# Kernel tuning notes

Measured on AMD Instinct MI355X. Metric: run time of the kernel, lower is better.

The kernel has to match this reference:

```python
import jax, jax.numpy as jnp
import numpy as np

B, H, M_DIM, K, N = 4, 8, 2048, 2048, 64
NNZ = B * H * M_DIM * 64


def setup_inputs() -> dict:
    key = jax.random.key(0)
    k_val, k_b, k_bh, k_m, k_k = jax.random.split(key, 5)
    values = jax.random.normal(k_val, (NNZ,), dtype=jnp.float32)
    b = jax.random.normal(k_b, (B, H, K, N), dtype=jnp.float32)
    idx_bh = jax.random.randint(k_bh, (NNZ,), 0, B * H, dtype=jnp.int32)
    idx_m = jax.random.randint(k_m, (NNZ,), 0, M_DIM, dtype=jnp.int32)
    idx_k = jax.random.randint(k_k, (NNZ,), 0, K, dtype=jnp.int32)
    return {"values": values, "b": b, "idx_bh": idx_bh, "idx_m": idx_m,
            "idx_k": idx_k, "M": M_DIM}


def reference(values, b, idx_bh, idx_m, idx_k, M):
    # Batched sparse-dense matmul: out[b,h,m,:] = sum_k A[b,h,m,k] * b[b,h,k,:]
    # A is in COO form over flattened batch-head dim: (idx_bh, idx_m, idx_k, values).
    Bd, Hd, Kd, Nd = b.shape
    b_flat = b.reshape(Bd * Hd, Kd, Nd)             # [BH, K, N]
    # gather the dense rows each nonzero touches, scale by the sparse value
    gathered = values[:, None] * b_flat[idx_bh, idx_k]  # [nnz, N]
    # scatter-add into output rows (flat segment id = bh*M + m)
    seg = idx_bh * M + idx_m
    out = jax.ops.segment_sum(gathered, seg, num_segments=Bd * Hd * M)  # [BH*M, N]
    return out.reshape(Bd, Hd, M, Nd)
```

## Files before the change

kernel.cpp:

```cpp
#include <hip/hip_runtime.h>

constexpr int N_COLS = 64;
constexpr int K_DIM  = 2048;
constexpr int M_DIM  = 2048;
constexpr int SEGS   = 32 * 2048;
constexpr int NBUCK  = 512;
constexpr int SEG_PER_BUCK = SEGS / NBUCK;
constexpr int PART_T = 512;
constexpr int PART_E = 16;
constexpr int TILE   = PART_T * PART_E;
constexpr int CAP2   = 8192;
constexpr int CSTR   = 16;
constexpr int OVL_CAP = 640;
constexpr size_t OVFCNT_OFF = 32768;
constexpr size_t OVFBUF_OFF = 40960;
constexpr int OVF_GCAP = (int)((524288 - OVFBUF_OFF) / 8);

struct Pair { float v; int k; };

__global__ void spmm_coo_atomic(const float* __restrict__ values,
                                const float* __restrict__ b,
                                const int*   __restrict__ idx_bh,
                                const int*   __restrict__ idx_m,
                                const int*   __restrict__ idx_k,
                                float*       __restrict__ out,
                                int nnz) {
    long long gid = (long long)blockIdx.x * blockDim.x + threadIdx.x;
    int nz   = (int)(gid >> 6);
    int lane = (int)(gid & 63);
    if (nz >= nnz) return;
    float bval = b[((size_t)idx_bh[nz] * K_DIM + idx_k[nz]) * N_COLS + lane];
    atomicAdd(&out[((size_t)idx_bh[nz] * M_DIM + idx_m[nz]) * N_COLS + lane],
              values[nz] * bval);
}

__global__ __launch_bounds__(PART_T)
void partition512(const float* __restrict__ values,
                  const int*   __restrict__ idx_bh,
                  const int*   __restrict__ idx_m,
                  const int*   __restrict__ idx_k,
                  int*  __restrict__ cursor,
                  int*  __restrict__ ovfcnt,
                  Pair* __restrict__ ovf,
                  Pair* __restrict__ packed, int nnz) {
    __shared__ int2 ebuf[TILE];
    __shared__ int lcount[NBUCK];
    __shared__ int sc[NBUCK];
    __shared__ int lstart[NBUCK];
    __shared__ int total_s;

    int t = threadIdx.x;
    lcount[t] = 0;
    __syncthreads();

    int e0 = blockIdx.x * TILE + t * PART_E;
    float v[PART_E];
    int   pk[PART_E];
    short bkt[PART_E];
    short rnk[PART_E];

    if (e0 + PART_E <= nnz) {
        const float4* vv4 = (const float4*)(values + e0);
        const int4*   bh4 = (const int4*)(idx_bh + e0);
        const int4*   mm4 = (const int4*)(idx_m + e0);
        const int4*   kk4 = (const int4*)(idx_k + e0);
        #pragma unroll
        for (int q = 0; q < PART_E / 4; ++q) {
            float4 vq = vv4[q];
            int4   bq = bh4[q], mq = mm4[q], kq = kk4[q];
            int s0 = bq.x * M_DIM + mq.x;
            int s1 = bq.y * M_DIM + mq.y;
            int s2 = bq.z * M_DIM + mq.z;
            int s3 = bq.w * M_DIM + mq.w;
            int b0 = s0 >> 7, b1 = s1 >> 7, b2 = s2 >> 7, b3 = s3 >> 7;
            v[4*q+0]=vq.x; pk[4*q+0]=(kq.x<<8)|((s0&127)<<19)|(b0&0xFF)|((b0>>8)<<26);
            bkt[4*q+0]=(short)b0; rnk[4*q+0]=(short)atomicAdd(&lcount[b0],1);
            v[4*q+1]=vq.y; pk[4*q+1]=(kq.y<<8)|((s1&127)<<19)|(b1&0xFF)|((b1>>8)<<26);
            bkt[4*q+1]=(short)b1; rnk[4*q+1]=(short)atomicAdd(&lcount[b1],1);
            v[4*q+2]=vq.z; pk[4*q+2]=(kq.z<<8)|((s2&127)<<19)|(b2&0xFF)|((b2>>8)<<26);
            bkt[4*q+2]=(short)b2; rnk[4*q+2]=(short)atomicAdd(&lcount[b2],1);
            v[4*q+3]=vq.w; pk[4*q+3]=(kq.w<<8)|((s3&127)<<19)|(b3&0xFF)|((b3>>8)<<26);
            bkt[4*q+3]=(short)b3; rnk[4*q+3]=(short)atomicAdd(&lcount[b3],1);
        }
    } else {
        #pragma unroll
        for (int i = 0; i < PART_E; ++i) {
            int e = e0 + i;
            if (e < nnz) {
                int seg = idx_bh[e] * M_DIM + idx_m[e];
                int bu  = seg >> 7;
                v[i]  = values[e];
                pk[i] = (idx_k[e] << 8) | ((seg & 127) << 19)
                      | (bu & 0xFF) | ((bu >> 8) << 26);
                bkt[i] = (short)bu;
                rnk[i] = (short)atomicAdd(&lcount[bu], 1);
            } else bkt[i] = -1;
        }
    }
    __syncthreads();

    int c = lcount[t];
    int sbase = (c > 0) ? atomicAdd(&cursor[t * CSTR], c) : 0;

    sc[t] = c;
    __syncthreads();
    for (int d = 1; d < NBUCK; d <<= 1) {
        int x = (t >= d) ? sc[t - d] : 0;
        __syncthreads();
        sc[t] += x;
        __syncthreads();
    }
    int ls = sc[t] - c;
    lstart[t] = ls;
    if (t == NBUCK - 1) total_s = sc[t];
    __syncthreads();
    sc[t] = sbase - ls;

    #pragma unroll
    for (int i = 0; i < PART_E; ++i) {
        if (bkt[i] >= 0)
            ebuf[lstart[bkt[i]] + rnk[i]] = make_int2(__float_as_int(v[i]), pk[i]);
    }
    __syncthreads();

    int total = total_s;
    for (int p = t; p < total; p += PART_T) {
        int2 e = ebuf[p];
        int bu = (e.y & 0xFF) | ((e.y >> 18) & 0x100);
        int gpos = sc[bu] + p;
        if (gpos < CAP2) {
            *(int2*)&packed[(size_t)bu * CAP2 + gpos] = e;
        } else {
            int o = atomicAdd(ovfcnt, 1);
            if (o < OVF_GCAP) *(int2*)&ovf[o] = e;
        }
    }
}

__global__ __launch_bounds__(1024)
void sort_accum(const Pair* __restrict__ packed,
                const int*  __restrict__ cursor,
                const int*  __restrict__ ovfcnt,
                const Pair* __restrict__ ovf,
                const float* __restrict__ b,
                float* __restrict__ out) {
    __shared__ int2 ps[CAP2 + OVL_CAP + 8];
    __shared__ int2 ovl[OVL_CAP];
    __shared__ int h[SEG_PER_BUCK];
    __shared__ int cur[SEG_PER_BUCK];
    __shared__ int ovl_n;

    int t = threadIdx.x;
    int i   = blockIdx.x;
    int bkt = (i & 7) * 64 + (i >> 3);
    int cnt = cursor[bkt * CSTR];
    int L = cnt;
    if (L < 0)    L = 0;
    if (L > CAP2) L = CAP2;

    if (t < SEG_PER_BUCK) h[t] = 0;
    if (t == 0) ovl_n = 0;
    __syncthreads();

    const int2* src = (const int2*)(packed + (size_t)bkt * CAP2);
    int2 reg[8];
    #pragma unroll
    for (int q = 0; q < 8; ++q) {
        int idx = t + q * 1024;
        if (idx < L) {
            reg[q] = src[idx];
            atomicAdd(&h[(reg[q].y >> 19) & 127], 1);
        }
    }
    int ovfN = ovfcnt[0];
    if (ovfN > OVF_GCAP) ovfN = OVF_GCAP;
    const int2* osrc = (const int2*)ovf;
    for (int o = t; o < ovfN; o += 1024) {
        int2 e = osrc[o];
        int eb = (e.y & 0xFF) | ((e.y >> 18) & 0x100);
        if (eb == bkt) {
            int pos = atomicAdd(&ovl_n, 1);
            if (pos < OVL_CAP) {
                ovl[pos] = e;
                atomicAdd(&h[(e.y >> 19) & 127], 1);
            }
        }
    }
    __syncthreads();

    for (int d = 1; d < SEG_PER_BUCK; d <<= 1) {
        int x = 0;
        if (t < SEG_PER_BUCK && t >= d) x = h[t - d];
        __syncthreads();
        if (t < SEG_PER_BUCK && t >= d) h[t] += x;
        __syncthreads();
    }
    if (t < SEG_PER_BUCK) cur[t] = (t == 0) ? 0 : h[t - 1];
    __syncthreads();

    #pragma unroll
    for (int q = 0; q < 8; ++q) {
        int idx = t + q * 1024;
        if (idx < L) {
            int pos = atomicAdd(&cur[(reg[q].y >> 19) & 127], 1);
            ps[pos] = make_int2(reg[q].y & 0x0007FF00, reg[q].x);
        }
    }
    int on = ovl_n; if (on > OVL_CAP) on = OVL_CAP;
    if (t < on) {
        int2 e = ovl[t];
        int pos = atomicAdd(&cur[(e.y >> 19) & 127], 1);
        ps[pos] = make_int2(e.y & 0x0007FF00, e.x);
    }
    __syncthreads();
    if (t < 8) ps[h[SEG_PER_BUCK - 1] + t] = make_int2(0, 0);
    __syncthreads();

    int lane = t & 63;
    int w    = t >> 6;
    int bh   = bkt >> 4;
    const char* bbyte = (const char*)(b + ((size_t)bh << 17));
    size_t obase = ((size_t)bkt << 13);

    for (int s = w * 8; s < w * 8 + 8; ++s) {
        int js = (s == 0) ? 0 : h[s - 1];
        int je = h[s];
        float a0 = 0.f, a1 = 0.f, a2 = 0.f, a3 = 0.f;
        int j = js;
        for (; j + 8 <= je; j += 8) {
            int2 e0 = ps[j+0], e1 = ps[j+1], e2 = ps[j+2], e3 = ps[j+3];
            int2 e4 = ps[j+4], e5 = ps[j+5], e6 = ps[j+6], e7 = ps[j+7];
            const float* r0 = (const float*)(bbyte + __builtin_amdgcn_readfirstlane(e0.x));
            const float* r1 = (const float*)(bbyte + __builtin_amdgcn_readfirstlane(e1.x));
            const float* r2 = (const float*)(bbyte + __builtin_amdgcn_readfirstlane(e2.x));
            const float* r3 = (const float*)(bbyte + __builtin_amdgcn_readfirstlane(e3.x));
            const float* r4 = (const float*)(bbyte + __builtin_amdgcn_readfirstlane(e4.x));
            const float* r5 = (const float*)(bbyte + __builtin_amdgcn_readfirstlane(e5.x));
            const float* r6 = (const float*)(bbyte + __builtin_amdgcn_readfirstlane(e6.x));
            const float* r7 = (const float*)(bbyte + __builtin_amdgcn_readfirstlane(e7.x));
            float b0 = r0[lane], b1 = r1[lane], b2 = r2[lane], b3 = r3[lane];
            float b4 = r4[lane], b5 = r5[lane], b6 = r6[lane], b7 = r7[lane];
            a0 += __int_as_float(e0.y) * b0; a1 += __int_as_float(e1.y) * b1;
            a2 += __int_as_float(e2.y) * b2; a3 += __int_as_float(e3.y) * b3;
            a0 += __int_as_float(e4.y) * b4; a1 += __int_as_float(e5.y) * b5;
            a2 += __int_as_float(e6.y) * b6; a3 += __int_as_float(e7.y) * b7;
        }
        if (j < je) {
            int2 e0 = ps[j+0], e1 = ps[j+1], e2 = ps[j+2], e3 = ps[j+3];
            int2 e4 = ps[j+4], e5 = ps[j+5], e6 = ps[j+6], e7 = ps[j+7];
            const float* r0 = (const float*)(bbyte + __builtin_amdgcn_readfirstlane(e0.x));
            const float* r1 = (const float*)(bbyte + __builtin_amdgcn_readfirstlane(e1.x));
            const float* r2 = (const float*)(bbyte + __builtin_amdgcn_readfirstlane(e2.x));
            const float* r3 = (const float*)(bbyte + __builtin_amdgcn_readfirstlane(e3.x));
            const float* r4 = (const float*)(bbyte + __builtin_amdgcn_readfirstlane(e4.x));
            const float* r5 = (const float*)(bbyte + __builtin_amdgcn_readfirstlane(e5.x));
            const float* r6 = (const float*)(bbyte + __builtin_amdgcn_readfirstlane(e6.x));
            const float* r7 = (const float*)(bbyte + __builtin_amdgcn_readfirstlane(e7.x));
            float b0 = r0[lane], b1 = r1[lane], b2 = r2[lane], b3 = r3[lane];
            float b4 = r4[lane], b5 = r5[lane], b6 = r6[lane], b7 = r7[lane];
            float v0 = (j+0 < je) ? __int_as_float(e0.y) : 0.f;
            float v1 = (j+1 < je) ? __int_as_float(e1.y) : 0.f;
            float v2 = (j+2 < je) ? __int_as_float(e2.y) : 0.f;
            float v3 = (j+3 < je) ? __int_as_float(e3.y) : 0.f;
            float v4 = (j+4 < je) ? __int_as_float(e4.y) : 0.f;
            float v5 = (j+5 < je) ? __int_as_float(e5.y) : 0.f;
            float v6 = (j+6 < je) ? __int_as_float(e6.y) : 0.f;
            float v7 = (j+7 < je) ? __int_as_float(e7.y) : 0.f;
            a0 += v0 * b0; a1 += v1 * b1; a2 += v2 * b2; a3 += v3 * b3;
            a0 += v4 * b4; a1 += v5 * b5; a2 += v6 * b6; a3 += v7 * b7;
        }
        out[obase + ((size_t)s << 6) + lane] = (a0 + a1) + (a2 + a3);
    }
}

extern "C" void kernel_launch(void* const* d_in, const int* in_sizes, int n_in,
                              void* d_out, int out_size, void* d_ws, size_t ws_size,
                              hipStream_t stream) {
    const float* values = (const float*)d_in[0];
    const float* b      = (const float*)d_in[1];
    const int*   idx_bh = (const int*)d_in[2];
    const int*   idx_m  = (const int*)d_in[3];
    const int*   idx_k  = (const int*)d_in[4];
    float*       out    = (float*)d_out;
    const int    nnz    = in_sizes[0];

    const size_t packed_off = 512 * 1024;
    const size_t need = packed_off + (size_t)NBUCK * CAP2 * sizeof(Pair);

    int*  cursor = (int*)d_ws;
    int*  ovfcnt = (int*)((char*)d_ws + OVFCNT_OFF);
    Pair* ovfbuf = (Pair*)((char*)d_ws + OVFBUF_OFF);
    Pair* packed = (Pair*)((char*)d_ws + packed_off);

    const int nblk = (nnz + TILE - 1) / TILE;

    if (ws_size >= need) {
        hipMemsetAsync(d_ws, 0, OVFBUF_OFF, stream);
        partition512<<<nblk, PART_T, 0, stream>>>(values, idx_bh, idx_m, idx_k,
                                                  cursor, ovfcnt, ovfbuf, packed, nnz);
        sort_accum<<<NBUCK, 1024, 0, stream>>>(packed, cursor, ovfcnt, ovfbuf, b, out);
    } else {
        hipMemsetAsync(d_out, 0, (size_t)out_size * sizeof(float), stream);
        long long total = (long long)nnz * N_COLS;
        spmm_coo_atomic<<<(unsigned)((total + 255) / 256), 256, 0, stream>>>(
            values, b, idx_bh, idx_m, idx_k, out, nnz);
    }
}
```

Baseline: 194.1 us.

## Pack sparse entries into 32 bits and gather B as bf16

New measurement: 200.6 us. +3.3%, slower.

```diff
diff --git a/kernel.cpp b/kernel.cpp
--- a/kernel.cpp
+++ b/kernel.cpp
@@ -15,6 +15,8 @@
 constexpr size_t OVFCNT_OFF = 32768;
 constexpr size_t OVFBUF_OFF = 40960;
 constexpr int OVF_GCAP = (int)((524288 - OVFBUF_OFF) / 8);
+constexpr size_t BBF_OFF    = 524288;
+constexpr size_t PACKED_OFF = BBF_OFF + 8388608;
 
 struct Pair { float v; int k; };
 
@@ -34,6 +36,22 @@
               values[nz] * bval);
 }
 
+__global__ __launch_bounds__(256)
+void conv_b(const float* __restrict__ b, unsigned int* __restrict__ bbf, int n8) {
+    int i = blockIdx.x * 256 + threadIdx.x;
+    if (i >= n8) return;
+    const float4* s = (const float4*)b + (size_t)i * 2;
+    float4 x = s[0], y = s[1];
+    auto cv = [](float a, float c) {
+        unsigned ua = __float_as_uint(a), uc = __float_as_uint(c);
+        ua = (ua + 0x7FFFu + ((ua >> 16) & 1u)) >> 16;
+        uc = (uc + 0x7FFFu + ((uc >> 16) & 1u)) >> 16;
+        return ua | (uc << 16);
+    };
+    uint4 r = make_uint4(cv(x.x, x.y), cv(x.z, x.w), cv(y.x, y.y), cv(y.z, y.w));
+    *(uint4*)(bbf + (size_t)i * 4) = r;
+}
+
 __global__ __launch_bounds__(PART_T)
 void partition512(const float* __restrict__ values,
                   const int*   __restrict__ idx_bh,
@@ -41,9 +59,10 @@
                   const int*   __restrict__ idx_k,
                   int*  __restrict__ cursor,
                   int*  __restrict__ ovfcnt,
-                  Pair* __restrict__ ovf,
-                  Pair* __restrict__ packed, int nnz) {
-    __shared__ int2 ebuf[TILE];
+                  int2* __restrict__ ovf,
+                  int*  __restrict__ packed, int nnz) {
+    __shared__ int ebuf[TILE];
+    __shared__ unsigned short bbuf[TILE];
     __shared__ int lcount[NBUCK];
     __shared__ int sc[NBUCK];
     __shared__ int lstart[NBUCK];
@@ -54,33 +73,36 @@
     __syncthreads();
 
     int e0 = blockIdx.x * TILE + t * PART_E;
-    float v[PART_E];
     int   pk[PART_E];
     short bkt[PART_E];
     short rnk[PART_E];
 
+    auto enc = [](int vb, int k, int seg) {
+        return (int)(((unsigned)(vb + 0x20000) & 0xFFFC0000u) | ((unsigned)k << 7)
+                     | ((unsigned)seg & 127u));
+    };
+
     if (e0 + PART_E <= nnz) {
-        const float4* vv4 = (const float4*)(values + e0);
-        const int4*   bh4 = (const int4*)(idx_bh + e0);
-        const int4*   mm4 = (const int4*)(idx_m + e0);
-        const int4*   kk4 = (const int4*)(idx_k + e0);
+        const int4* vv4 = (const int4*)(values + e0);
+        const int4* bh4 = (const int4*)(idx_bh + e0);
+        const int4* mm4 = (const int4*)(idx_m + e0);
+        const int4* kk4 = (const int4*)(idx_k + e0);
         #pragma unroll
         for (int q = 0; q < PART_E / 4; ++q) {
-            float4 vq = vv4[q];
-            int4   bq = bh4[q], mq = mm4[q], kq = kk4[q];
+            int4 vq = vv4[q];
+            int4 bq = bh4[q], mq = mm4[q], kq = kk4[q];
             int s0 = bq.x * M_DIM + mq.x;
             int s1 = bq.y * M_DIM + mq.y;
             int s2 = bq.z * M_DIM + mq.z;
             int s3 = bq.w * M_DIM + mq.w;
-            int b0 = s0 >> 7, b1 = s1 >> 7, b2 = s2 >> 7, b3 = s3 >> 7;
-            v[4*q+0]=vq.x; pk[4*q+0]=(kq.x<<8)|((s0&127)<<19)|(b0&0xFF)|((b0>>8)<<26);
-            bkt[4*q+0]=(short)b0; rnk[4*q+0]=(short)atomicAdd(&lcount[b0],1);
-            v[4*q+1]=vq.y; pk[4*q+1]=(kq.y<<8)|((s1&127)<<19)|(b1&0xFF)|((b1>>8)<<26);
-            bkt[4*q+1]=(short)b1; rnk[4*q+1]=(short)atomicAdd(&lcount[b1],1);
-            v[4*q+2]=vq.z; pk[4*q+2]=(kq.z<<8)|((s2&127)<<19)|(b2&0xFF)|((b2>>8)<<26);
-            bkt[4*q+2]=(short)b2; rnk[4*q+2]=(short)atomicAdd(&lcount[b2],1);
-            v[4*q+3]=vq.w; pk[4*q+3]=(kq.w<<8)|((s3&127)<<19)|(b3&0xFF)|((b3>>8)<<26);
-            bkt[4*q+3]=(short)b3; rnk[4*q+3]=(short)atomicAdd(&lcount[b3],1);
+            pk[4*q+0]=enc(vq.x,kq.x,s0); bkt[4*q+0]=(short)(s0>>7);
+            rnk[4*q+0]=(short)atomicAdd(&lcount[s0>>7],1);
+            pk[4*q+1]=enc(vq.y,kq.y,s1); bkt[4*q+1]=(short)(s1>>7);
+            rnk[4*q+1]=(short)atomicAdd(&lcount[s1>>7],1);
+            pk[4*q+2]=enc(vq.z,kq.z,s2); bkt[4*q+2]=(short)(s2>>7);
+            rnk[4*q+2]=(short)atomicAdd(&lcount[s2>>7],1);
+            pk[4*q+3]=enc(vq.w,kq.w,s3); bkt[4*q+3]=(short)(s3>>7);
+            rnk[4*q+3]=(short)atomicAdd(&lcount[s3>>7],1);
         }
     } else {
         #pragma unroll
@@ -89,9 +111,7 @@
             if (e < nnz) {
                 int seg = idx_bh[e] * M_DIM + idx_m[e];
                 int bu  = seg >> 7;
-                v[i]  = values[e];
-                pk[i] = (idx_k[e] << 8) | ((seg & 127) << 19)
-                      | (bu & 0xFF) | ((bu >> 8) << 26);
+                pk[i]  = enc(__float_as_int(values[e]), idx_k[e], seg);
                 bkt[i] = (short)bu;
                 rnk[i] = (short)atomicAdd(&lcount[bu], 1);
             } else bkt[i] = -1;
@@ -118,34 +138,37 @@
 
     #pragma unroll
     for (int i = 0; i < PART_E; ++i) {
-        if (bkt[i] >= 0)
-            ebuf[lstart[bkt[i]] + rnk[i]] = make_int2(__float_as_int(v[i]), pk[i]);
+        if (bkt[i] >= 0) {
+            int p = lstart[bkt[i]] + rnk[i];
+            ebuf[p] = pk[i];
+            bbuf[p] = (unsigned short)bkt[i];
+        }
     }
     __syncthreads();
 
     int total = total_s;
     for (int p = t; p < total; p += PART_T) {
-        int2 e = ebuf[p];
-        int bu = (e.y & 0xFF) | ((e.y >> 18) & 0x100);
+        int e  = ebuf[p];
+        int bu = bbuf[p];
         int gpos = sc[bu] + p;
         if (gpos < CAP2) {
-            *(int2*)&packed[(size_t)bu * CAP2 + gpos] = e;
+            packed[(size_t)bu * CAP2 + gpos] = e;
         } else {
             int o = atomicAdd(ovfcnt, 1);
-            if (o < OVF_GCAP) *(int2*)&ovf[o] = e;
+            if (o < OVF_GCAP) ovf[o] = make_int2(e, bu);
         }
     }
 }
 
 __global__ __launch_bounds__(1024)
-void sort_accum(const Pair* __restrict__ packed,
+void sort_accum(const int*  __restrict__ packed,
                 const int*  __restrict__ cursor,
                 const int*  __restrict__ ovfcnt,
-                const Pair* __restrict__ ovf,
-                const float* __restrict__ b,
+                const int2* __restrict__ ovf,
+                const unsigned short* __restrict__ bbf,
                 float* __restrict__ out) {
-    __shared__ int2 ps[CAP2 + OVL_CAP + 8];
-    __shared__ int2 ovl[OVL_CAP];
+    __shared__ int ps[CAP2 + OVL_CAP + 8];
+    __shared__ int ovl[OVL_CAP];
     __shared__ int h[SEG_PER_BUCK];
     __shared__ int cur[SEG_PER_BUCK];
     __shared__ int ovl_n;
@@ -162,27 +185,24 @@
     if (t == 0) ovl_n = 0;
     __syncthreads();
 
-    const int2* src = (const int2*)(packed + (size_t)bkt * CAP2);
-    int2 reg[8];
+    const int4* src4 = (const int4*)(packed + (size_t)bkt * CAP2);
+    int4 ra = src4[t * 2];
+    int4 rb = src4[t * 2 + 1];
+    int er[8] = { ra.x, ra.y, ra.z, ra.w, rb.x, rb.y, rb.z, rb.w };
+    int base8 = t * 8;
     #pragma unroll
-    for (int q = 0; q < 8; ++q) {
-        int idx = t + q * 1024;
-        if (idx < L) {
-            reg[q] = src[idx];
-            atomicAdd(&h[(reg[q].y >> 19) & 127], 1);
-        }
-    }
+    for (int q = 0; q < 8; ++q)
+        if (base8 + q < L) atomicAdd(&h[er[q] & 127], 1);
+
     int ovfN = ovfcnt[0];
     if (ovfN > OVF_GCAP) ovfN = OVF_GCAP;
-    const int2* osrc = (const int2*)ovf;
     for (int o = t; o < ovfN; o += 1024) {
-        int2 e = osrc[o];
-        int eb = (e.y & 0xFF) | ((e.y >> 18) & 0x100);
-        if (eb == bkt) {
+        int2 e = ovf[o];
+        if (e.y == bkt) {
             int pos = atomicAdd(&ovl_n, 1);
             if (pos < OVL_CAP) {
-                ovl[pos] = e;
-                atomicAdd(&h[(e.y >> 19) & 127], 1);
+                ovl[pos] = e.x;
+                atomicAdd(&h[e.x & 127], 1);
             }
         }
     }
@@ -200,27 +220,27 @@
 
     #pragma unroll
     for (int q = 0; q < 8; ++q) {
-        int idx = t + q * 1024;
-        if (idx < L) {
-            int pos = atomicAdd(&cur[(reg[q].y >> 19) & 127], 1);
-            ps[pos] = make_int2(reg[q].y & 0x0007FF00, reg[q].x);
+        if (base8 + q < L) {
+            int pos = atomicAdd(&cur[er[q] & 127], 1);
+            ps[pos] = er[q];
         }
     }
     int on = ovl_n; if (on > OVL_CAP) on = OVL_CAP;
     if (t < on) {
-        int2 e = ovl[t];
-        int pos = atomicAdd(&cur[(e.y >> 19) & 127], 1);
-        ps[pos] = make_int2(e.y & 0x0007FF00, e.x);
-    }
-    __syncthreads();
-    if (t < 8) ps[h[SEG_PER_BUCK - 1] + t] = make_int2(0, 0);
+        int e = ovl[t];
+        int pos = atomicAdd(&cur[e & 127], 1);
+        ps[pos] = e;
+    }
+    __syncthreads();
+    if (t < 8) ps[h[SEG_PER_BUCK - 1] + t] = 0;
     __syncthreads();
 
     int lane = t & 63;
     int w    = t >> 6;
     int bh   = bkt >> 4;
-    const char* bbyte = (const char*)(b + ((size_t)bh << 17));
+    const char* bb = (const char*)bbf + ((size_t)bh << 18);
     size_t obase = ((size_t)bkt << 13);
+    int lb = lane * 2;
 
     for (int s = w * 8; s < w * 8 + 8; ++s) {
         int js = (s == 0) ? 0 : h[s - 1];
@@ -228,46 +248,64 @@
         float a0 = 0.f, a1 = 0.f, a2 = 0.f, a3 = 0.f;
         int j = js;
         for (; j + 8 <= je; j += 8) {
-            int2 e0 = ps[j+0], e1 = ps[j+1], e2 = ps[j+2], e3 = ps[j+3];
-            int2 e4 = ps[j+4], e5 = ps[j+5], e6 = ps[j+6], e7 = ps[j+7];
-            const float* r0 = (const float*)(bbyte + __builtin_amdgcn_readfirstlane(e0.x));
-            const float* r1 = (const float*)(bbyte + __builtin_amdgcn_readfirstlane(e1.x));
-            const float* r2 = (const float*)(bbyte + __builtin_amdgcn_readfirstlane(e2.x));
-            const float* r3 = (const float*)(bbyte + __builtin_amdgcn_readfirstlane(e3.x));
-            const float* r4 = (const float*)(bbyte + __builtin_amdgcn_readfirstlane(e4.x));
-            const float* r5 = (const float*)(bbyte + __builtin_amdgcn_readfirstlane(e5.x));
-            const float* r6 = (const float*)(bbyte + __builtin_amdgcn_readfirstlane(e6.x));
-            const float* r7 = (const float*)(bbyte + __builtin_amdgcn_readfirstlane(e7.x));
-            float b0 = r0[lane], b1 = r1[lane], b2 = r2[lane], b3 = r3[lane];
-            float b4 = r4[lane], b5 = r5[lane], b6 = r6[lane], b7 = r7[lane];
-            a0 += __int_as_float(e0.y) * b0; a1 += __int_as_float(e1.y) * b1;
-            a2 += __int_as_float(e2.y) * b2; a3 += __int_as_float(e3.y) * b3;
-            a0 += __int_as_float(e4.y) * b4; a1 += __int_as_float(e5.y) * b5;
-            a2 += __int_as_float(e6.y) * b6; a3 += __int_as_float(e7.y) * b7;
+            int s0 = __builtin_amdgcn_readfirstlane(ps[j+0]);
+            int s1 = __builtin_amdgcn_readfirstlane(ps[j+1]);
+            int s2 = __builtin_amdgcn_readfirstlane(ps[j+2]);
+            int s3 = __builtin_amdgcn_readfirstlane(ps[j+3]);
+            int s4 = __builtin_amdgcn_readfirstlane(ps[j+4]);
+            int s5 = __builtin_amdgcn_readfirstlane(ps[j+5]);
+            int s6 = __builtin_amdgcn_readfirstlane(ps[j+6]);
+            int s7 = __builtin_amdgcn_readfirstlane(ps[j+7]);
+            unsigned short u0 = *(const unsigned short*)(bb + (s0 & 0x3FF80) + lb);
+            unsigned short u1 = *(const unsigned short*)(bb + (s1 & 0x3FF80) + lb);
+            unsigned short u2 = *(const unsigned short*)(bb + (s2 & 0x3FF80) + lb);
+            unsigned short u3 = *(const unsigned short*)(bb + (s3 & 0x3FF80) + lb);
+            unsigned short u4 = *(const unsigned short*)(bb + (s4 & 0x3FF80) + lb);
+            unsigned short u5 = *(const unsigned short*)(bb + (s5 & 0x3FF80) + lb);
+            unsigned short u6 = *(const unsigned short*)(bb + (s6 & 0x3FF80) + lb);
+            unsigned short u7 = *(const unsigned short*)(bb + (s7 & 0x3FF80) + lb);
+            a0 += __int_as_float(s0 & (int)0xFFFC0000) * __int_as_float((int)u0 << 16);
+            a1 += __int_as_float(s1 & (int)0xFFFC0000) * __int_as_float((int)u1 << 16);
+            a2 += __int_as_float(s2 & (int)0xFFFC0000) * __int_as_float((int)u2 << 16);
+            a3 += __int_as_float(s3 & (int)0xFFFC0000) * __int_as_float((int)u3 << 16);
+            a0 += __int_as_float(s4 & (int)0xFFFC0000) * __int_as_float((int)u4 << 16);
+            a1 += __int_as_float(s5 & (int)0xFFFC0000) * __int_as_float((int)u5 << 16);
+            a2 += __int_as_float(s6 & (int)0xFFFC0000) * __int_as_float((int)u6 << 16);
+            a3 += __int_as_float(s7 & (int)0xFFFC0000) * __int_as_float((int)u7 << 16);
         }
         if (j < je) {
-            int2 e0 = ps[j+0], e1 = ps[j+1], e2 = ps[j+2], e3 = ps[j+3];
-            int2 e4 = ps[j+4], e5 = ps[j+5], e6 = ps[j+6], e7 = ps[j+7];
-            const float* r0 = (const float*)(bbyte + __builtin_amdgcn_readfirstlane(e0.x));
-            const float* r1 = (const float*)(bbyte + __builtin_amdgcn_readfirstlane(e1.x));
-            const float* r2 = (const float*)(bbyte + __builtin_amdgcn_readfirstlane(e2.x));
-            const float* r3 = (const float*)(bbyte + __builtin_amdgcn_readfirstlane(e3.x));
-            const float* r4 = (const float*)(bbyte + __builtin_amdgcn_readfirstlane(e4.x));
-            const float* r5 = (const float*)(bbyte + __builtin_amdgcn_readfirstlane(e5.x));
-            const float* r6 = (const float*)(bbyte + __builtin_amdgcn_readfirstlane(e6.x));
-            const float* r7 = (const float*)(bbyte + __builtin_amdgcn_readfirstlane(e7.x));
-            float b0 = r0[lane], b1 = r1[lane], b2 = r2[lane], b3 = r3[lane];
-            float b4 = r4[lane], b5 = r5[lane], b6 = r6[lane], b7 = r7[lane];
-            float v0 = (j+0 < je) ? __int_as_float(e0.y) : 0.f;
-            float v1 = (j+1 < je) ? __int_as_float(e1.y) : 0.f;
-            float v2 = (j+2 < je) ? __int_as_float(e2.y) : 0.f;
-            float v3 = (j+3 < je) ? __int_as_float(e3.y) : 0.f;
-            float v4 = (j+4 < je) ? __int_as_float(e4.y) : 0.f;
-            float v5 = (j+5 < je) ? __int_as_float(e5.y) : 0.f;
-            float v6 = (j+6 < je) ? __int_as_float(e6.y) : 0.f;
-            float v7 = (j+7 < je) ? __int_as_float(e7.y) : 0.f;
-            a0 += v0 * b0; a1 += v1 * b1; a2 += v2 * b2; a3 += v3 * b3;
-            a0 += v4 * b4; a1 += v5 * b5; a2 += v6 * b6; a3 += v7 * b7;
+            int s0 = __builtin_amdgcn_readfirstlane(ps[j+0]);
+            int s1 = __builtin_amdgcn_readfirstlane(ps[j+1]);
+            int s2 = __builtin_amdgcn_readfirstlane(ps[j+2]);
+            int s3 = __builtin_amdgcn_readfirstlane(ps[j+3]);
+            int s4 = __builtin_amdgcn_readfirstlane(ps[j+4]);
+            int s5 = __builtin_amdgcn_readfirstlane(ps[j+5]);
+            int s6 = __builtin_amdgcn_readfirstlane(ps[j+6]);
+            int s7 = __builtin_amdgcn_readfirstlane(ps[j+7]);
+            unsigned short u0 = *(const unsigned short*)(bb + (s0 & 0x3FF80) + lb);
+            unsigned short u1 = *(const unsigned short*)(bb + (s1 & 0x3FF80) + lb);
+            unsigned short u2 = *(const unsigned short*)(bb + (s2 & 0x3FF80) + lb);
+            unsigned short u3 = *(const unsigned short*)(bb + (s3 & 0x3FF80) + lb);
+            unsigned short u4 = *(const unsigned short*)(bb + (s4 & 0x3FF80) + lb);
+            unsigned short u5 = *(const unsigned short*)(bb + (s5 & 0x3FF80) + lb);
+            unsigned short u6 = *(const unsigned short*)(bb + (s6 & 0x3FF80) + lb);
+            unsigned short u7 = *(const unsigned short*)(bb + (s7 & 0x3FF80) + lb);
+            float v0 = (j+0 < je) ? __int_as_float(s0 & (int)0xFFFC0000) : 0.f;
+            float v1 = (j+1 < je) ? __int_as_float(s1 & (int)0xFFFC0000) : 0.f;
+            float v2 = (j+2 < je) ? __int_as_float(s2 & (int)0xFFFC0000) : 0.f;
+            float v3 = (j+3 < je) ? __int_as_float(s3 & (int)0xFFFC0000) : 0.f;
+            float v4 = (j+4 < je) ? __int_as_float(s4 & (int)0xFFFC0000) : 0.f;
+            float v5 = (j+5 < je) ? __int_as_float(s5 & (int)0xFFFC0000) : 0.f;
+            float v6 = (j+6 < je) ? __int_as_float(s6 & (int)0xFFFC0000) : 0.f;
+            float v7 = (j+7 < je) ? __int_as_float(s7 & (int)0xFFFC0000) : 0.f;
+            a0 += v0 * __int_as_float((int)u0 << 16);
+            a1 += v1 * __int_as_float((int)u1 << 16);
+            a2 += v2 * __int_as_float((int)u2 << 16);
+            a3 += v3 * __int_as_float((int)u3 << 16);
+            a0 += v4 * __int_as_float((int)u4 << 16);
+            a1 += v5 * __int_as_float((int)u5 << 16);
+            a2 += v6 * __int_as_float((int)u6 << 16);
+            a3 += v7 * __int_as_float((int)u7 << 16);
         }
         out[obase + ((size_t)s << 6) + lane] = (a0 + a1) + (a2 + a3);
     }
@@ -284,21 +322,24 @@
     float*       out    = (float*)d_out;
     const int    nnz    = in_sizes[0];
 
-    const size_t packed_off = 512 * 1024;
-    const size_t need = packed_off + (size_t)NBUCK * CAP2 * sizeof(Pair);
+    const size_t need = PACKED_OFF + (size_t)NBUCK * CAP2 * sizeof(int);
 
     int*  cursor = (int*)d_ws;
     int*  ovfcnt = (int*)((char*)d_ws + OVFCNT_OFF);
-    Pair* ovfbuf = (Pair*)((char*)d_ws + OVFBUF_OFF);
-    Pair* packed = (Pair*)((char*)d_ws + packed_off);
+    int2* ovfbuf = (int2*)((char*)d_ws + OVFBUF_OFF);
+    unsigned int*   bbf    = (unsigned int*)((char*)d_ws + BBF_OFF);
+    int*  packed = (int*)((char*)d_ws + PACKED_OFF);
 
     const int nblk = (nnz + TILE - 1) / TILE;
+    const int nb8  = (4 * 8 * K_DIM * N_COLS) / 8;
 
     if (ws_size >= need) {
         hipMemsetAsync(d_ws, 0, OVFBUF_OFF, stream);
+        conv_b<<<nb8 / 256, 256, 0, stream>>>(b, bbf, nb8);
         partition512<<<nblk, PART_T, 0, stream>>>(values, idx_bh, idx_m, idx_k,
                                                   cursor, ovfcnt, ovfbuf, packed, nnz);
-        sort_accum<<<NBUCK, 1024, 0, stream>>>(packed, cursor, ovfcnt, ovfbuf, b, out);
+        sort_accum<<<NBUCK, 1024, 0, stream>>>(packed, cursor, ovfcnt, ovfbuf,
+                                               (const unsigned short*)bbf, out);
     } else {
         hipMemsetAsync(d_out, 0, (size_t)out_size * sizeof(float), stream);
         long long total = (long long)nnz * N_COLS;
```
